# Performance work log

Hardware: AMD Instinct MI355X
Metric: run time of the kernel (lower is better)

The kernel has to match this reference:

```python
import jax, jax.numpy as jnp
import numpy as np

EMBED_DIM = 1024
HEAD_SIZE = 64
BATCH = 8
SEQ = 2048


def setup_inputs() -> dict:
    key = jax.random.key(0)
    k1, k2, k3, k4 = jax.random.split(key, 4)
    x = jax.random.normal(k1, (BATCH, SEQ, EMBED_DIM), dtype=jnp.float32)
    # Dense(use_bias=False) kernels: [in, out]
    scale = 1.0 / np.sqrt(EMBED_DIM)
    Wq = jax.random.normal(k2, (EMBED_DIM, HEAD_SIZE), dtype=jnp.float32) * scale
    Wk = jax.random.normal(k3, (EMBED_DIM, HEAD_SIZE), dtype=jnp.float32) * scale
    Wv = jax.random.normal(k4, (EMBED_DIM, HEAD_SIZE), dtype=jnp.float32) * scale
    return {"x": x, "Wq": Wq, "Wk": Wk, "Wv": Wv}


def reference(x, Wq, Wk, Wv):
    B, S, E = x.shape
    q = jnp.einsum("bse,eh->bsh", x, Wq)
    k = jnp.einsum("bse,eh->bsh", x, Wk)
    v = jnp.einsum("bse,eh->bsh", x, Wv)
    # scores scaled by embedding_dim**-0.5 (as in the original code)
    w = jnp.einsum("bqh,bkh->bqk", q, k) * (E ** -0.5)
    causal = jnp.tril(jnp.ones((S, S), dtype=bool))  # True on/below diag
    w = jnp.where(causal, w, -jnp.inf)
    w = jax.nn.softmax(w, axis=-1)
    # dropout is identity at inference
    return jnp.einsum("bqk,bkh->bqh", w, v)
```

## Files before the change

kernel.cpp:

```cpp
#include <hip/hip_runtime.h>
#include <hip/hip_bf16.h>


#define BATCH 8
#define SEQ   2048
#define EMB   1024
#define HD    64
#define ROWS  (BATCH*SEQ)
#define BK    64
#define NKT   (EMB / BK)
#define NSPLIT 4

typedef __attribute__((ext_vector_type(8))) short short8;
typedef __attribute__((ext_vector_type(4))) float floatx4;

static __device__ __forceinline__ short f2bf(float f) {
  union { __hip_bfloat16 h; short s; } u;
  u.h = __float2bfloat16(f);
  return u.s;
}

static __device__ __forceinline__ short8 pack8(float4 u, float4 v) {
  short8 r;
  r[0] = f2bf(u.x); r[1] = f2bf(u.y); r[2] = f2bf(u.z); r[3] = f2bf(u.w);
  r[4] = f2bf(v.x); r[5] = f2bf(v.y); r[6] = f2bf(v.z); r[7] = f2bf(v.w);
  return r;
}

__global__ __launch_bounds__(256) void wt_kernel(
    const float* __restrict__ Wq, const float* __restrict__ Wk,
    const float* __restrict__ Wv, short* __restrict__ Wd) {
  const int id = blockIdx.x * 256 + threadIdx.x;
  const int lane = id & 63;
  const int ks = (id >> 6) & 1;
  const int id2 = id >> 7;
  const int nt = id2 % 12;
  const int kt = id2 / 12;
  const int lo = lane & 15, quad = lane >> 4;
  const int np = nt * 16 + lo;
  const float* __restrict__ W = (np < 64) ? Wq : ((np < 128) ? Wk : Wv);
  const int n = np & 63;
  const int k0 = kt * BK + (4 * ks + quad) * 8;
  short8 o;
#pragma unroll
  for (int u = 0; u < 8; ++u) o[u] = f2bf(W[(size_t)(k0 + u) * HD + n]);
  *(short8*)(Wd + (size_t)id * 8) = o;
}

__global__ __launch_bounds__(256, 2) void proj_kernel(
    const float* __restrict__ x, const short* __restrict__ Wd,
    short* __restrict__ qb, short* __restrict__ kb_, short* __restrict__ vtb) {
  __shared__ __align__(16) short Ab[2][32 * 64];

  const int t = threadIdx.x, lane = t & 63, w = t >> 6;
  const int lo = lane & 15, quad = lane >> 4;
  const int e = lo & 7;
  const int m0 = blockIdx.x * 32;

  const int srow = t >> 3, sc = t & 7;
  const float* sgp = x + (size_t)(m0 + srow) * EMB + sc * 8;
  const int sslot = srow * 64 + ((sc ^ (srow & 7)) << 3);

  const short* bgp = Wd + (size_t)(w * 3) * 1024 + lane * 8;

  floatx4 acc[2][3];
#pragma unroll
  for (int mf = 0; mf < 2; ++mf)
#pragma unroll
    for (int j = 0; j < 3; ++j) acc[mf][j] = (floatx4){0.f, 0.f, 0.f, 0.f};

  short8 bcur[3][2], bnxt[3][2];
  float4 ra, rb;

  auto LOADA = [&](int kt) {
    const float* p = sgp + kt * BK;
    ra = *(const float4*)(p);
    rb = *(const float4*)(p + 4);
  };
  auto LOAD_B = [&](short8 (&bf)[3][2], int kt) {
    const short* bg = bgp + (size_t)kt * 12288;
#pragma unroll
    for (int j = 0; j < 3; ++j)
#pragma unroll
      for (int ks = 0; ks < 2; ++ks)
        bf[j][ks] = *(const short8*)(bg + j * 1024 + ks * 512);
  };

  LOADA(0);
  LOAD_B(bcur, 0);
  *(short8*)(&Ab[0][sslot]) = pack8(ra, rb);
  __syncthreads();

  int buf = 0;
  for (int kt = 0; kt < NKT; ++kt) {
    const bool more = (kt + 1 < NKT);
    if (more) { LOADA(kt + 1); LOAD_B(bnxt, kt + 1); }
    short8 af[2][2];
#pragma unroll
    for (int mf = 0; mf < 2; ++mf)
#pragma unroll
      for (int ks = 0; ks < 2; ++ks)
        af[mf][ks] = *(const short8*)(
            &Ab[buf][(mf * 16 + lo) * 64 + (((4 * ks + quad) ^ e) << 3)]);
#pragma unroll
    for (int ks = 0; ks < 2; ++ks)
#pragma unroll
      for (int j = 0; j < 3; ++j) {
        acc[0][j] = __builtin_amdgcn_mfma_f32_16x16x32_bf16(af[0][ks], bcur[j][ks], acc[0][j], 0, 0, 0);
        acc[1][j] = __builtin_amdgcn_mfma_f32_16x16x32_bf16(af[1][ks], bcur[j][ks], acc[1][j], 0, 0, 0);
      }
    if (more) {
      *(short8*)(&Ab[buf ^ 1][sslot]) = pack8(ra, rb);
#pragma unroll
      for (int j = 0; j < 3; ++j)
#pragma unroll
        for (int ks = 0; ks < 2; ++ks) bcur[j][ks] = bnxt[j][ks];
    }
    __syncthreads();
    buf ^= 1;
  }

  const int bb = m0 >> 11;
  const int sbase = (m0 & (SEQ - 1)) + quad * 4;
#pragma unroll
  for (int mf = 0; mf < 2; ++mf) {
    const int rowb = m0 + mf * 16 + quad * 4;
#pragma unroll
    for (int j = 0; j < 3; ++j) {
      const int nt = w * 3 + j;
      const floatx4 v = acc[mf][j];
      if (nt < 4) {
#pragma unroll
        for (int r = 0; r < 4; ++r)
          qb[(size_t)(rowb + r) * HD + nt * 16 + lo] = f2bf(v[r] * 0.03125f);
      } else if (nt < 8) {
#pragma unroll
        for (int r = 0; r < 4; ++r)
          kb_[(size_t)(rowb + r) * HD + (nt - 4) * 16 + lo] = f2bf(v[r]);
      } else {
        const int col = (nt - 8) * 16 + lo;
        short4 sv = make_short4(f2bf(v[0]), f2bf(v[1]), f2bf(v[2]), f2bf(v[3]));
        *(short4*)(vtb + ((size_t)bb * HD + col) * SEQ + sbase + mf * 16) = sv;
      }
    }
  }
}

#define PSTR 40

__global__ __launch_bounds__(256, 6) void attn_kernel(
    const short* __restrict__ qb, const short* __restrict__ kb,
    const short* __restrict__ vtb, float* __restrict__ pacc,
    float* __restrict__ plsum) {
  __shared__ __align__(16) short Ps[4][16 * PSTR];
  __shared__ __align__(16) floatx4 Red[2][5][64];

  const int b = blockIdx.y;
  const int bx = blockIdx.x;
  const int qx = bx >> 2;
  const int sp = bx & 3;
  const int q0 = qx * 32;
  const int t = threadIdx.x, lane = t & 63, w = t >> 6;
  const int wr = w >> 1, wk = w & 1;
  const int lo = lane & 15, quad = lane >> 4;

  const int niter = q0 / 64 + 1;
  const int it0 = (sp * niter) >> 2;
  const int it1 = ((sp + 1) * niter) >> 2;

  const short* qp = qb + ((size_t)b * SEQ + q0 + wr * 16 + lo) * HD + quad * 8;
  const short8 qf0 = *(const short8*)(qp);
  const short8 qf1 = *(const short8*)(qp + 32);

  const short* __restrict__ kgb = kb + (size_t)b * SEQ * HD;
  const short* __restrict__ vgb = vtb + (size_t)b * HD * SEQ;
  const short* kbase = kgb + (size_t)(wk * 32 + lo) * HD + quad * 8;
  const short* vbase = vgb + (size_t)lo * SEQ + wk * 32 + quad * 8;

  floatx4 acc[4];
  float lsum[4] = {0.f, 0.f, 0.f, 0.f};
#pragma unroll
  for (int nt = 0; nt < 4; ++nt) acc[nt] = (floatx4){0.f, 0.f, 0.f, 0.f};

  short* Pw = Ps[w];
  const int rowb = q0 + wr * 16 + quad * 4;

  for (int it = it0; it < it1; ++it) {
    const int j0 = it * 64;
    short8 kf[2][2], vf[4];
    {
      const short* kp = kbase + (size_t)j0 * HD;
#pragma unroll
      for (int n2 = 0; n2 < 2; ++n2) {
        kf[n2][0] = *(const short8*)(kp + n2 * (16 * HD));
        kf[n2][1] = *(const short8*)(kp + n2 * (16 * HD) + 32);
      }
      const short* vp = vbase + j0;
#pragma unroll
      for (int nt = 0; nt < 4; ++nt)
        vf[nt] = *(const short8*)(vp + (size_t)(nt * 16) * SEQ);
    }

    floatx4 s0 = (floatx4){0.f, 0.f, 0.f, 0.f};
    floatx4 s1 = (floatx4){0.f, 0.f, 0.f, 0.f};
    __builtin_amdgcn_s_setprio(1);
    s0 = __builtin_amdgcn_mfma_f32_16x16x32_bf16(qf0, kf[0][0], s0, 0, 0, 0);
    s0 = __builtin_amdgcn_mfma_f32_16x16x32_bf16(qf1, kf[0][1], s0, 0, 0, 0);
    s1 = __builtin_amdgcn_mfma_f32_16x16x32_bf16(qf0, kf[1][0], s1, 0, 0, 0);
    s1 = __builtin_amdgcn_mfma_f32_16x16x32_bf16(qf1, kf[1][1], s1, 0, 0, 0);
    __builtin_amdgcn_s_setprio(0);

    const bool diag = (j0 + 64 > q0);
#pragma unroll
    for (int r = 0; r < 4; ++r) {
      float e0 = __expf(s0[r]);
      float e1 = __expf(s1[r]);
      if (diag) {
        const int key0 = j0 + wk * 32 + lo;
        e0 = (key0 <= rowb + r) ? e0 : 0.f;
        e1 = (key0 + 16 <= rowb + r) ? e1 : 0.f;
      }
      lsum[r] += e0 + e1;
      Pw[(quad * 4 + r) * PSTR + lo] = f2bf(e0);
      Pw[(quad * 4 + r) * PSTR + 16 + lo] = f2bf(e1);
    }
    const short8 pf = *(const short8*)(&Pw[lo * PSTR + quad * 8]);
    __builtin_amdgcn_s_setprio(1);
#pragma unroll
    for (int nt = 0; nt < 4; ++nt)
      acc[nt] = __builtin_amdgcn_mfma_f32_16x16x32_bf16(pf, vf[nt], acc[nt], 0, 0, 0);
    __builtin_amdgcn_s_setprio(0);
  }

#pragma unroll
  for (int d = 1; d < 16; d <<= 1) {
#pragma unroll
    for (int r = 0; r < 4; ++r) lsum[r] += __shfl_xor(lsum[r], d);
  }

  if (wk == 1) {
#pragma unroll
    for (int nt = 0; nt < 4; ++nt) Red[wr][nt][lane] = acc[nt];
    Red[wr][4][lane] = (floatx4){lsum[0], lsum[1], lsum[2], lsum[3]};
  }
  __syncthreads();
  if (wk == 0) {
    const floatx4 lp = Red[wr][4][lane];
#pragma unroll
    for (int nt = 0; nt < 4; ++nt) {
      const floatx4 o = acc[nt] + Red[wr][nt][lane];
#pragma unroll
      for (int r = 0; r < 4; ++r)
        pacc[(((size_t)b * SEQ + rowb + r) * NSPLIT + sp) * HD + nt * 16 + lo] = o[r];
    }
    if (lo == 0) {
#pragma unroll
      for (int r = 0; r < 4; ++r)
        plsum[((size_t)b * SEQ + rowb + r) * NSPLIT + sp] = lsum[r] + lp[r];
    }
  }
}

__global__ __launch_bounds__(256) void comb_kernel(
    const float* __restrict__ pacc, const float* __restrict__ plsum,
    float* __restrict__ out) {
  const int idx = blockIdx.x * 256 + threadIdx.x;
  const int row = idx >> 4;
  const int h4 = (idx & 15) << 2;
  const float* pa = pacc + (size_t)row * (NSPLIT * HD) + h4;
  float4 s = make_float4(0.f, 0.f, 0.f, 0.f);
  float d = 0.f;
#pragma unroll
  for (int sp = 0; sp < NSPLIT; ++sp) {
    const float4 v = *(const float4*)(pa + sp * HD);
    s.x += v.x; s.y += v.y; s.z += v.z; s.w += v.w;
    d += plsum[(size_t)row * NSPLIT + sp];
  }
  const float inv = 1.0f / d;
  float4 o = make_float4(s.x * inv, s.y * inv, s.z * inv, s.w * inv);
  *(float4*)(out + (size_t)row * HD + h4) = o;
}

extern "C" void kernel_launch(void* const* d_in, const int* in_sizes, int n_in,
                              void* d_out, int out_size, void* d_ws, size_t ws_size,
                              hipStream_t stream) {
  const float* x  = (const float*)d_in[0];
  const float* Wq = (const float*)d_in[1];
  const float* Wk = (const float*)d_in[2];
  const float* Wv = (const float*)d_in[3];
  float* out = (float*)d_out;
  short* ws = (short*)d_ws;
  short* qbp = ws;
  short* kbp = ws + (size_t)ROWS * HD;
  short* vtp = ws + (size_t)2 * ROWS * HD;
  short* Wd  = ws + (size_t)3 * ROWS * HD;
  float* pacc  = (float*)(ws + (size_t)3 * ROWS * HD + 196608);
  float* plsum = pacc + (size_t)ROWS * NSPLIT * HD;

  wt_kernel<<<dim3(96), 256, 0, stream>>>(Wq, Wk, Wv, Wd);
  proj_kernel<<<dim3(ROWS / 32), 256, 0, stream>>>(x, Wd, qbp, kbp, vtp);
  attn_kernel<<<dim3(64 * NSPLIT, BATCH), 256, 0, stream>>>(qbp, kbp, vtp, pacc, plsum);
  comb_kernel<<<dim3(ROWS * 16 / 256), 256, 0, stream>>>(pacc, plsum, out);
}
```

Baseline: 163.2 us.

## Restructure attention work split: per-wave key interleave, longest-first scheduling, register prefetch

Each block now handles 16 query rows. Its four waves stride through 32-key chunks in interleaved fashion and write separate partials, which removes the LDS reduction and __syncthreads. Query tiles are launched in reverse order so the longest causal rows start first, and K/V fragments for the next chunk are prefetched into registers while the current chunk computes. The trade-off is more blocks, each with less query reuse of loaded K/V. Register pressure also rises, and the launch bound is relaxed from 6 to 4 blocks.

New measurement: 152.6 us. 1.07x faster.

```diff
diff --git a/kernel.cpp b/kernel.cpp
--- a/kernel.cpp
+++ b/kernel.cpp
@@ -148,34 +148,28 @@
 
 #define PSTR 40
 
-__global__ __launch_bounds__(256, 6) void attn_kernel(
+__global__ __launch_bounds__(256, 4) void attn_kernel(
     const short* __restrict__ qb, const short* __restrict__ kb,
     const short* __restrict__ vtb, float* __restrict__ pacc,
     float* __restrict__ plsum) {
   __shared__ __align__(16) short Ps[4][16 * PSTR];
-  __shared__ __align__(16) floatx4 Red[2][5][64];
-
-  const int b = blockIdx.y;
+
   const int bx = blockIdx.x;
-  const int qx = bx >> 2;
-  const int sp = bx & 3;
-  const int q0 = qx * 32;
-  const int t = threadIdx.x, lane = t & 63, w = t >> 6;
-  const int wr = w >> 1, wk = w & 1;
+  const int qt = 127 - (bx >> 3);
+  const int b = bx & 7;
+  const int w = threadIdx.x >> 6;
+  const int sp = w;
+  const int lane = threadIdx.x & 63;
   const int lo = lane & 15, quad = lane >> 4;
-
-  const int niter = q0 / 64 + 1;
-  const int it0 = (sp * niter) >> 2;
-  const int it1 = ((sp + 1) * niter) >> 2;
-
-  const short* qp = qb + ((size_t)b * SEQ + q0 + wr * 16 + lo) * HD + quad * 8;
+  const int q0 = qt * 16;
+  const int niter = (qt >> 1) + 1;
+
+  const short* qp = qb + ((size_t)b * SEQ + q0 + lo) * HD + quad * 8;
   const short8 qf0 = *(const short8*)(qp);
   const short8 qf1 = *(const short8*)(qp + 32);
 
   const short* __restrict__ kgb = kb + (size_t)b * SEQ * HD;
   const short* __restrict__ vgb = vtb + (size_t)b * HD * SEQ;
-  const short* kbase = kgb + (size_t)(wk * 32 + lo) * HD + quad * 8;
-  const short* vbase = vgb + (size_t)lo * SEQ + wk * 32 + quad * 8;
 
   floatx4 acc[4];
   float lsum[4] = {0.f, 0.f, 0.f, 0.f};
@@ -183,24 +177,29 @@
   for (int nt = 0; nt < 4; ++nt) acc[nt] = (floatx4){0.f, 0.f, 0.f, 0.f};
 
   short* Pw = Ps[w];
-  const int rowb = q0 + wr * 16 + quad * 4;
-
-  for (int it = it0; it < it1; ++it) {
-    const int j0 = it * 64;
-    short8 kf[2][2], vf[4];
-    {
-      const short* kp = kbase + (size_t)j0 * HD;
-#pragma unroll
-      for (int n2 = 0; n2 < 2; ++n2) {
-        kf[n2][0] = *(const short8*)(kp + n2 * (16 * HD));
-        kf[n2][1] = *(const short8*)(kp + n2 * (16 * HD) + 32);
-      }
-      const short* vp = vbase + j0;
-#pragma unroll
-      for (int nt = 0; nt < 4; ++nt)
-        vf[nt] = *(const short8*)(vp + (size_t)(nt * 16) * SEQ);
-    }
-
+  const int rowq = q0 + quad * 4;
+
+  const short* kp = kgb + (size_t)lo * HD + quad * 8 + (size_t)sp * 32 * HD;
+  const short* vp = vgb + (size_t)lo * SEQ + quad * 8 + sp * 32;
+
+  short8 kf[2][2], vf[4];
+  auto LOADK = [&]() {
+#pragma unroll
+    for (int kt2 = 0; kt2 < 2; ++kt2)
+#pragma unroll
+      for (int ks = 0; ks < 2; ++ks)
+        kf[kt2][ks] = *(const short8*)(kp + kt2 * 16 * HD + ks * 32);
+  };
+  auto LOADV = [&]() {
+#pragma unroll
+    for (int nt = 0; nt < 4; ++nt)
+      vf[nt] = *(const short8*)(vp + (size_t)nt * 16 * SEQ);
+  };
+
+  int it = sp;
+  if (it < niter) { LOADK(); LOADV(); }
+  for (; it < niter; it += NSPLIT) {
+    const int j0 = it * 32;
     floatx4 s0 = (floatx4){0.f, 0.f, 0.f, 0.f};
     floatx4 s1 = (floatx4){0.f, 0.f, 0.f, 0.f};
     __builtin_amdgcn_s_setprio(1);
@@ -209,16 +208,17 @@
     s1 = __builtin_amdgcn_mfma_f32_16x16x32_bf16(qf0, kf[1][0], s1, 0, 0, 0);
     s1 = __builtin_amdgcn_mfma_f32_16x16x32_bf16(qf1, kf[1][1], s1, 0, 0, 0);
     __builtin_amdgcn_s_setprio(0);
-
-    const bool diag = (j0 + 64 > q0);
+    const bool more = (it + NSPLIT < niter);
+    kp += NSPLIT * 32 * HD;
+    if (more) LOADK();
+    const bool diag = (j0 + 32 > q0);
 #pragma unroll
     for (int r = 0; r < 4; ++r) {
       float e0 = __expf(s0[r]);
       float e1 = __expf(s1[r]);
       if (diag) {
-        const int key0 = j0 + wk * 32 + lo;
-        e0 = (key0 <= rowb + r) ? e0 : 0.f;
-        e1 = (key0 + 16 <= rowb + r) ? e1 : 0.f;
+        e0 = (j0 + lo <= rowq + r) ? e0 : 0.f;
+        e1 = (j0 + 16 + lo <= rowq + r) ? e1 : 0.f;
       }
       lsum[r] += e0 + e1;
       Pw[(quad * 4 + r) * PSTR + lo] = f2bf(e0);
@@ -230,6 +230,8 @@
     for (int nt = 0; nt < 4; ++nt)
       acc[nt] = __builtin_amdgcn_mfma_f32_16x16x32_bf16(pf, vf[nt], acc[nt], 0, 0, 0);
     __builtin_amdgcn_s_setprio(0);
+    vp += NSPLIT * 32;
+    if (more) LOADV();
   }
 
 #pragma unroll
@@ -238,26 +240,17 @@
     for (int r = 0; r < 4; ++r) lsum[r] += __shfl_xor(lsum[r], d);
   }
 
-  if (wk == 1) {
-#pragma unroll
-    for (int nt = 0; nt < 4; ++nt) Red[wr][nt][lane] = acc[nt];
-    Red[wr][4][lane] = (floatx4){lsum[0], lsum[1], lsum[2], lsum[3]};
-  }
-  __syncthreads();
-  if (wk == 0) {
-    const floatx4 lp = Red[wr][4][lane];
-#pragma unroll
-    for (int nt = 0; nt < 4; ++nt) {
-      const floatx4 o = acc[nt] + Red[wr][nt][lane];
-#pragma unroll
-      for (int r = 0; r < 4; ++r)
-        pacc[(((size_t)b * SEQ + rowb + r) * NSPLIT + sp) * HD + nt * 16 + lo] = o[r];
-    }
-    if (lo == 0) {
-#pragma unroll
-      for (int r = 0; r < 4; ++r)
-        plsum[((size_t)b * SEQ + rowb + r) * NSPLIT + sp] = lsum[r] + lp[r];
-    }
+#pragma unroll
+  for (int nt = 0; nt < 4; ++nt) {
+#pragma unroll
+    for (int r = 0; r < 4; ++r)
+      pacc[(((size_t)b * SEQ + rowq + r) * NSPLIT + sp) * HD + nt * 16 + lo] =
+          acc[nt][r];
+  }
+  if (lo == 0) {
+#pragma unroll
+    for (int r = 0; r < 4; ++r)
+      plsum[((size_t)b * SEQ + rowq + r) * NSPLIT + sp] = lsum[r];
   }
 }
 
@@ -299,6 +292,6 @@
 
   wt_kernel<<<dim3(96), 256, 0, stream>>>(Wq, Wk, Wv, Wd);
   proj_kernel<<<dim3(ROWS / 32), 256, 0, stream>>>(x, Wd, qbp, kbp, vtp);
-  attn_kernel<<<dim3(64 * NSPLIT, BATCH), 256, 0, stream>>>(qbp, kbp, vtp, pacc, plsum);
+  attn_kernel<<<dim3(128 * 8), 256, 0, stream>>>(qbp, kbp, vtp, pacc, plsum);
   comb_kernel<<<dim3(ROWS * 16 / 256), 256, 0, stream>>>(pacc, plsum, out);
 }
```
